# Optimization experiments

Measured on AMD Instinct MI355X. Metric: run time of the kernel, lower is better.

Reference implementation:

```python
import jax, jax.numpy as jnp
import numpy as np

HOP = 128
NFFT = 256
SR = 16000
EPS = 1e-7
MIN_DB = -80.0


def _a_weighting_db():
    # librosa.fft_frequencies + librosa.A_weighting (min_db=-80), computed statically in numpy
    f = np.fft.rfftfreq(NFFT, d=1.0 / SR)  # [NFFT//2+1]
    c = np.array([12194.217, 20.598997, 107.65265, 737.86223]) ** 2.0
    f2 = f ** 2.0
    w = 2.0 + 20.0 * (
        np.log10(c[0])
        + 2.0 * np.log10(np.maximum(f2, 1e-30))
        - np.log10(f2 + c[0])
        - np.log10(f2 + c[1])
        - 0.5 * np.log10(f2 + c[2])
        - 0.5 * np.log10(f2 + c[3])
    )
    return np.maximum(w, MIN_DB).astype(np.float32)


def _loudness(x):
    # x: [B, C, T] -> channel mean -> librosa-style centered STFT (hann, reflect pad)
    x = jnp.mean(x, axis=1)  # [B, T]
    T = x.shape[1]
    pad = NFFT // 2
    xp = jnp.pad(x, ((0, 0), (pad, pad)), mode='reflect')  # [B, T+NFFT]
    n_frames = 1 + T // HOP
    idx = jnp.arange(n_frames)[:, None] * HOP + jnp.arange(NFFT)[None, :]  # [F, NFFT]
    frames = xp[:, idx]  # [B, F, NFFT]
    # periodic hann window (scipy fftbins=True, librosa default)
    win = (0.5 - 0.5 * jnp.cos(2.0 * jnp.pi * jnp.arange(NFFT) / NFFT)).astype(x.dtype)
    spec = jnp.fft.rfft(frames * win, axis=-1)  # [B, F, NFFT//2+1] complex
    log_mag = jnp.log(jnp.abs(spec) + EPS)  # [B, F, NFREQ]
    aw = jnp.asarray(_a_weighting_db())  # [NFREQ]
    # mean over frequency axis, then trailing singleton like original unsqueeze(-1)
    loud = jnp.mean(log_mag + aw[None, None, :], axis=-1)  # [B, F]
    return loud[..., None].astype(jnp.float32)


def setup_inputs() -> dict:
    key = jax.random.key(0)
    x = jax.random.normal(key, (64, 1, 640000), dtype=jnp.float32)
    return {"x": x}


def reference(x):
    return _loudness(x)
```

## Files before the change

### kernel.cpp

```cpp
#include <hip/hip_runtime.h>
#include <math.h>

#define HOP 128
#define T_LEN 640000
#define N_FRAMES 5001
#define N_PAIRS 2501
#define NB 64
#define GPB 16

#define RE_SLOT 18
#define RE_GRP  164
#define IM_SLOT 18
#define IM_GRP  132

typedef float v2f __attribute__((ext_vector_type(2)));

static __device__ __forceinline__ v2f mk2(float a, float b) { v2f r; r.x = a; r.y = b; return r; }
static __device__ __forceinline__ v2f sp(float s) { v2f r; r.x = s; r.y = s; return r; }

static __device__ __forceinline__ float rsum16(float v) {
    v += __int_as_float(__builtin_amdgcn_update_dpp(0, __float_as_int(v), 0xB1, 0xF, 0xF, true));
    v += __int_as_float(__builtin_amdgcn_update_dpp(0, __float_as_int(v), 0x4E, 0xF, 0xF, true));
    v += __int_as_float(__builtin_amdgcn_update_dpp(0, __float_as_int(v), 0x141, 0xF, 0xF, true));
    v += __int_as_float(__builtin_amdgcn_update_dpp(0, __float_as_int(v), 0x140, 0xF, 0xF, true));
    return v;
}

__global__ __launch_bounds__(256) void setup_kernel(float* __restrict__ ws) {
    __shared__ float s_aw[132];
    const int tid = threadIdx.x;
    const float TP = 0.02454369260617026f;
    {
        const int w = tid >> 4, rr = tid & 15;
        float s, c;
        sincosf((float)(rr * w) * TP, &s, &c);
        ((v2f*)ws)[tid] = mk2(c, -s);
    }
    if (tid < 129) {
        const float LG2_10 = 0.30102999566398f;
        float fq = (float)tid * 62.5f;
        float f2 = fq * fq;
        const float a0 = 12194.217f * 12194.217f;
        const float a1 = 20.598997f * 20.598997f;
        const float a2 = 107.65265f * 107.65265f;
        const float a3 = 737.86223f * 737.86223f;
        float w = 2.0f + 20.0f * LG2_10 *
                  (__builtin_amdgcn_logf(a0) + 2.0f * __builtin_amdgcn_logf(fmaxf(f2, 1e-30f))
                 - __builtin_amdgcn_logf(f2 + a0) - __builtin_amdgcn_logf(f2 + a1)
                 - 0.5f * __builtin_amdgcn_logf(f2 + a2) - 0.5f * __builtin_amdgcn_logf(f2 + a3));
        s_aw[tid] = fmaxf(w, -80.0f);
    }
    __syncthreads();
    if (tid < 16) {
        float s = 0.f;
#pragma unroll
        for (int k2 = 0; k2 < 8; ++k2) s += s_aw[tid + 16 * k2];
        ws[512 + tid] = s;
        if (tid == 0) ws[528] = s_aw[128];
    }
}

__global__ __launch_bounds__(256) void loudness_kernel(const float* __restrict__ x,
                                                       float* __restrict__ out,
                                                       const float* __restrict__ ws) {
    constexpr float C16[16] = {
        1.0f,  0.9238795325112867f,  0.7071067811865476f,  0.3826834323650898f,
        0.0f, -0.3826834323650898f, -0.7071067811865476f, -0.9238795325112867f,
       -1.0f, -0.9238795325112867f, -0.7071067811865476f, -0.3826834323650898f,
        0.0f,  0.3826834323650898f,  0.7071067811865476f,  0.9238795325112867f};
    constexpr float S16[16] = {
        0.0f,  0.3826834323650898f,  0.7071067811865476f,  0.9238795325112867f,
        1.0f,  0.9238795325112867f,  0.7071067811865476f,  0.3826834323650898f,
        0.0f, -0.3826834323650898f, -0.7071067811865476f, -0.9238795325112867f,
       -1.0f, -0.9238795325112867f, -0.7071067811865476f, -0.3826834323650898f};
    const float R2  = 0.7071067811865476f;
    const float c1v = 0.9238795325112867f, s1v = 0.3826834323650898f;
    const float c3v = 0.3826834323650898f, s3v = 0.9238795325112867f;
    const float CP8 = 0.9238795325112867f, SP8 = 0.3826834323650898f;
    const float K2  = 1.8477590650225735f;

    __shared__ alignas(16) v2f s_re[16 * RE_GRP];
    __shared__ alignas(16) v2f s_im[16 * IM_GRP];
    __shared__ v2f s_twT[256];

    const int tid = threadIdx.x;
    const int g = tid >> 4;
    const int r = tid & 15;

    s_twT[tid] = ((const v2f*)ws)[tid];
    const float aw8r  = ws[512 + r];
    const float aw128 = ws[528];
    const v2f stp = ((const v2f*)ws)[16 + r];

    float win16[16];
    {
        float cm2 = stp.x;
        float cm1 = stp.x * CP8 + stp.y * SP8;
        win16[0] = 0.5f - 0.5f * cm2;
        win16[1] = 0.5f - 0.5f * cm1;
#pragma unroll
        for (int n = 2; n < 16; ++n) {
            const float c = K2 * cm1 - cm2;
            win16[n] = 0.5f - 0.5f * c;
            cm2 = cm1; cm1 = c;
        }
    }
    __syncthreads();

    const int gp = blockIdx.x * GPB + g;
    const int b  = gp / N_PAIRS;
    const int pp = gp - b * N_PAIRS;
    const int fA = 2 * pp;
    const int fB = (fA < 5000) ? fA + 1 : 5000;
    const int dB = (fB - fA) * HOP;
    const float* __restrict__ xb = x + (size_t)b * T_LEN;

    v2f xw[16];
    const int base = fA * HOP - HOP + r;
    if (pp >= 1 && pp <= 2499) {
        const float* __restrict__ xp = xb + base;
#pragma unroll
        for (int n2 = 0; n2 < 16; ++n2) {
            const int o = 16 * n2;
            xw[n2] = mk2(xp[o], xp[o + dB]) * sp(win16[n2]);
        }
    } else {
#pragma unroll
        for (int n2 = 0; n2 < 16; ++n2) {
            int jA = base + 16 * n2;
            int jB = jA + dB;
            jA = (jA < 0) ? -jA : jA;
            jA = (jA >= T_LEN) ? (2 * T_LEN - 2 - jA) : jA;
            jB = (jB < 0) ? -jB : jB;
            jB = (jB >= T_LEN) ? (2 * T_LEN - 2 - jB) : jB;
            xw[n2] = mk2(xb[jA], xb[jB]) * sp(win16[n2]);
        }
    }

    v2f pv[8], qv[8];
#pragma unroll
    for (int n = 1; n <= 7; ++n) { pv[n] = xw[n] + xw[16 - n]; qv[n] = xw[n] - xw[16 - n]; }
    const v2f bse = xw[0] + xw[8];
    const v2f d08 = xw[0] - xw[8];
    const v2f se  = pv[2] + pv[4] + pv[6];
    const v2f so  = pv[1] + pv[3] + pv[5] + pv[7];
    const v2f r0  = bse + se + so;
    const v2f r8  = bse + se - so;
    v2f rre[8], rim[8];
#pragma unroll
    for (int k1 = 1; k1 <= 7; ++k1) {
        v2f re = (k1 & 1) ? d08 : bse;
        v2f im = sp(0.f);
#pragma unroll
        for (int n = 1; n <= 7; ++n) {
            const int m = (k1 * n) & 15;
            re += pv[n] * sp(C16[m]);
            im -= qv[n] * sp(S16[m]);
        }
        rre[k1] = re;
        rim[k1] = im;
    }

    {
        v2f* __restrict__ reW = &s_re[g * RE_GRP + r];
        v2f* __restrict__ imW = &s_im[g * IM_GRP + r];
        reW[0] = r0;
#pragma unroll
        for (int k = 1; k <= 7; ++k) {
            reW[RE_SLOT * k] = rre[k];
            imW[IM_SLOT * (k - 1)] = rim[k];
        }
        reW[RE_SLOT * 8] = r8;
    }

    const int rp  = (r <= 8) ? r : 16 - r;
    const int rpi = (rp >= 1 && rp <= 7) ? (rp - 1) : 0;
    const float ysgn = (r == 0 || r == 8) ? 0.f : ((r < 8) ? 1.f : -1.f);
    const float4* __restrict__ reCol = (const float4*)&s_re[g * RE_GRP + RE_SLOT * rp];
    const float4* __restrict__ imCol = (const float4*)&s_im[g * IM_GRP + IM_SLOT * rpi];
    const v2f* __restrict__ twp = &s_twT[r];

    v2f bbx[16], bby[16];
#pragma unroll
    for (int j = 0; j < 8; ++j) {
        const float4 R4v = reCol[j];
        const float4 I4v = imCol[j];
        {
            const int w = 2 * j;
            const v2f tw = twp[16 * w];
            const v2f xx = mk2(R4v.x, R4v.y);
            const v2f yy = mk2(I4v.x, I4v.y) * sp(ysgn);
            bbx[w] = xx * sp(tw.x) - yy * sp(tw.y);
            bby[w] = xx * sp(tw.y) + yy * sp(tw.x);
        }
        {
            const int w = 2 * j + 1;
            const v2f tw = twp[16 * w];
            const v2f xx = mk2(R4v.z, R4v.w);
            const v2f yy = mk2(I4v.z, I4v.w) * sp(ysgn);
            bbx[w] = xx * sp(tw.x) - yy * sp(tw.y);
            bby[w] = xx * sp(tw.y) + yy * sp(tw.x);
        }
    }

#pragma unroll
    for (int j = 0; j < 8; ++j) {
        const v2f ux = bbx[j], uy = bby[j], vx = bbx[j + 8], vy = bby[j + 8];
        bbx[j] = ux + vx; bby[j] = uy + vy;
        const v2f dx = ux - vx, dy = uy - vy;
        v2f ox, oy;
        if      (j == 0) { ox = dx;                              oy = dy; }
        else if (j == 1) { ox =  dx * sp(c1v) + dy * sp(s1v);    oy =  dy * sp(c1v) - dx * sp(s1v); }
        else if (j == 2) { ox = (dx + dy) * sp(R2);              oy = (dy - dx) * sp(R2); }
        else if (j == 3) { ox =  dx * sp(c3v) + dy * sp(s3v);    oy =  dy * sp(c3v) - dx * sp(s3v); }
        else if (j == 4) { ox = dy;                              oy = sp(0.f) - dx; }
        else if (j == 5) { ox = dy * sp(s3v) - dx * sp(c3v);     oy = sp(0.f) - dy * sp(c3v) - dx * sp(s3v); }
        else if (j == 6) { ox = (dy - dx) * sp(R2);              oy = sp(0.f) - (dx + dy) * sp(R2); }
        else             { ox = dy * sp(s1v) - dx * sp(c1v);     oy = sp(0.f) - dy * sp(c1v) - dx * sp(s1v); }
        bbx[j + 8] = ox; bby[j + 8] = oy;
    }
#pragma unroll
    for (int h = 0; h <= 8; h += 8) {
#pragma unroll
        for (int j = 0; j < 4; ++j) {
            const v2f ux = bbx[h + j], uy = bby[h + j], vx = bbx[h + j + 4], vy = bby[h + j + 4];
            bbx[h + j] = ux + vx; bby[h + j] = uy + vy;
            const v2f dx = ux - vx, dy = uy - vy;
            v2f ox, oy;
            if      (j == 0) { ox = dx;                  oy = dy; }
            else if (j == 1) { ox = (dx + dy) * sp(R2);  oy = (dy - dx) * sp(R2); }
            else if (j == 2) { ox = dy;                  oy = sp(0.f) - dx; }
            else             { ox = (dy - dx) * sp(R2);  oy = sp(0.f) - (dx + dy) * sp(R2); }
            bbx[h + j + 4] = ox; bby[h + j + 4] = oy;
        }
    }
#pragma unroll
    for (int gg = 0; gg < 16; gg += 4) {
        {
            const v2f ux = bbx[gg], uy = bby[gg], vx = bbx[gg + 2], vy = bby[gg + 2];
            bbx[gg] = ux + vx;     bby[gg] = uy + vy;
            bbx[gg + 2] = ux - vx; bby[gg + 2] = uy - vy;
        }
        {
            const v2f ux = bbx[gg + 1], uy = bby[gg + 1], vx = bbx[gg + 3], vy = bby[gg + 3];
            bbx[gg + 1] = ux + vx; bby[gg + 1] = uy + vy;
            const v2f dx = ux - vx, dy = uy - vy;
            bbx[gg + 3] = dy; bby[gg + 3] = sp(0.f) - dx;
        }
    }

    const float HALF_LN2 = 0.34657359027997264f;
    v2f m2[8];
#pragma unroll
    for (int t = 0; t < 8; ++t) {
        const v2f Yx = bbx[2 * t] + bbx[2 * t + 1];
        const v2f Yy = bby[2 * t] + bby[2 * t + 1];
        m2[t] = Yx * Yx + Yy * Yy + sp(1e-14f);
    }
    const v2f P0 = m2[0] * m2[1], P1 = m2[2] * m2[3], P2 = m2[4] * m2[5], P3 = m2[6] * m2[7];
    const float lA = __builtin_amdgcn_logf(P0.x) + __builtin_amdgcn_logf(P1.x)
                   + __builtin_amdgcn_logf(P2.x) + __builtin_amdgcn_logf(P3.x);
    const float lB = __builtin_amdgcn_logf(P0.y) + __builtin_amdgcn_logf(P1.y)
                   + __builtin_amdgcn_logf(P2.y) + __builtin_amdgcn_logf(P3.y);
    v2f ssum = sp(HALF_LN2) * mk2(lA, lB) + sp(aw8r);

    const v2f d0 = bbx[0] - bbx[1];
    if (r == 0) {
        ssum += sp(HALF_LN2) * mk2(__builtin_amdgcn_logf(d0.x * d0.x + 1e-14f),
                                   __builtin_amdgcn_logf(d0.y * d0.y + 1e-14f))
              + sp(aw128);
    }

    ssum.x = rsum16(ssum.x);
    ssum.y = rsum16(ssum.y);

    if (r == 0) {
        out[b * N_FRAMES + fA] = ssum.x * (1.0f / 129.0f);
        out[b * N_FRAMES + fB] = ssum.y * (1.0f / 129.0f);
    }
}

extern "C" void kernel_launch(void* const* d_in, const int* in_sizes, int n_in,
                              void* d_out, int out_size, void* d_ws, size_t ws_size,
                              hipStream_t stream) {
    const float* x = (const float*)d_in[0];
    float* out = (float*)d_out;
    float* ws = (float*)d_ws;
    setup_kernel<<<1, 256, 0, stream>>>(ws);
    loudness_kernel<<<(NB * N_PAIRS) / GPB, 256, 0, stream>>>(x, out, ws);
}
```

Measured before the change: 55.48 us.

## Merge shared spectra buffers, fold twiddles in registers, swizzle blocks across XCDs

The block's twiddle table is dropped from shared memory. Twiddles are now applied before the transpose by a per-thread sincos and a rotation recurrence, and the twiddle for the high-half lanes is folded into constant C16/S16 multiplies. The real and imaginary spectra share one reused shared buffer written in two phases, which cuts the LDS footprint. A launch-bounds occupancy hint of 5 and an XCD-aware block-index swizzle for L2 locality are also added. The two-phase reuse and the recurrence-based twiddles may add numeric error and instruction dependencies, and the reuse has no __syncthreads between phases (each 16-lane group is assumed to sit within one wavefront).

```diff
diff --git a/kernel.cpp b/kernel.cpp
--- a/kernel.cpp
+++ b/kernel.cpp
@@ -7,11 +7,10 @@
 #define N_PAIRS 2501
 #define NB 64
 #define GPB 16
-
-#define RE_SLOT 18
-#define RE_GRP  164
-#define IM_SLOT 18
-#define IM_GRP  132
+#define NWG ((NB * N_PAIRS) / GPB)
+
+#define SLOT 18
+#define GRP  162
 
 typedef float v2f __attribute__((ext_vector_type(2)));
 
@@ -29,13 +28,6 @@
 __global__ __launch_bounds__(256) void setup_kernel(float* __restrict__ ws) {
     __shared__ float s_aw[132];
     const int tid = threadIdx.x;
-    const float TP = 0.02454369260617026f;
-    {
-        const int w = tid >> 4, rr = tid & 15;
-        float s, c;
-        sincosf((float)(rr * w) * TP, &s, &c);
-        ((v2f*)ws)[tid] = mk2(c, -s);
-    }
     if (tid < 129) {
         const float LG2_10 = 0.30102999566398f;
         float fq = (float)tid * 62.5f;
@@ -55,14 +47,14 @@
         float s = 0.f;
 #pragma unroll
         for (int k2 = 0; k2 < 8; ++k2) s += s_aw[tid + 16 * k2];
-        ws[512 + tid] = s;
-        if (tid == 0) ws[528] = s_aw[128];
+        ws[tid] = s;
+        if (tid == 0) ws[16] = s_aw[128];
     }
 }
 
-__global__ __launch_bounds__(256) void loudness_kernel(const float* __restrict__ x,
-                                                       float* __restrict__ out,
-                                                       const float* __restrict__ ws) {
+__global__ __launch_bounds__(256, 5) void loudness_kernel(const float* __restrict__ x,
+                                                          float* __restrict__ out,
+                                                          const float* __restrict__ ws) {
     constexpr float C16[16] = {
         1.0f,  0.9238795325112867f,  0.7071067811865476f,  0.3826834323650898f,
         0.0f, -0.3826834323650898f, -0.7071067811865476f, -0.9238795325112867f,
@@ -79,18 +71,34 @@
     const float CP8 = 0.9238795325112867f, SP8 = 0.3826834323650898f;
     const float K2  = 1.8477590650225735f;
 
-    __shared__ alignas(16) v2f s_re[16 * RE_GRP];
-    __shared__ alignas(16) v2f s_im[16 * IM_GRP];
-    __shared__ v2f s_twT[256];
+    __shared__ alignas(16) v2f s_sp[16 * GRP];
 
     const int tid = threadIdx.x;
     const int g = tid >> 4;
     const int r = tid & 15;
 
-    s_twT[tid] = ((const v2f*)ws)[tid];
-    const float aw8r  = ws[512 + r];
-    const float aw128 = ws[528];
-    const v2f stp = ((const v2f*)ws)[16 + r];
+    const int orig = blockIdx.x;
+    const int xcd = orig & 7, idx = orig >> 3;
+    const int q = NWG >> 3, rem = NWG & 7;
+    const int swz = (xcd < rem) ? xcd * (q + 1) + idx
+                                : rem * (q + 1) + (xcd - rem) * q + idx;
+
+    const int gp = swz * GPB + g;
+    const int b  = gp / N_PAIRS;
+    const int pp = gp - b * N_PAIRS;
+    const int fA = 2 * pp;
+    const int fB = (fA < 5000) ? fA + 1 : 5000;
+    const int dB = (fB - fA) * HOP;
+    const float* __restrict__ xb = x + (size_t)b * T_LEN;
+
+    v2f stp;
+    {
+        float s, c;
+        sincosf((float)r * 0.02454369260617026f, &s, &c);
+        stp = mk2(c, -s);
+    }
+    const float aw8r  = ws[r];
+    const float aw128 = ws[16];
 
     float win16[16];
     {
@@ -105,15 +113,6 @@
             cm2 = cm1; cm1 = c;
         }
     }
-    __syncthreads();
-
-    const int gp = blockIdx.x * GPB + g;
-    const int b  = gp / N_PAIRS;
-    const int pp = gp - b * N_PAIRS;
-    const int fA = 2 * pp;
-    const int fB = (fA < 5000) ? fA + 1 : 5000;
-    const int dB = (fB - fA) * HOP;
-    const float* __restrict__ xb = x + (size_t)b * T_LEN;
 
     v2f xw[16];
     const int base = fA * HOP - HOP + r;
@@ -161,45 +160,66 @@
         rim[k1] = im;
     }
 
+    v2f* __restrict__ wbase = &s_sp[g * GRP];
+    v2f Zim[9];
     {
-        v2f* __restrict__ reW = &s_re[g * RE_GRP + r];
-        v2f* __restrict__ imW = &s_im[g * IM_GRP + r];
-        reW[0] = r0;
-#pragma unroll
-        for (int k = 1; k <= 7; ++k) {
-            reW[RE_SLOT * k] = rre[k];
-            imW[IM_SLOT * (k - 1)] = rim[k];
-        }
-        reW[RE_SLOT * 8] = r8;
-    }
-
-    const int rp  = (r <= 8) ? r : 16 - r;
-    const int rpi = (rp >= 1 && rp <= 7) ? (rp - 1) : 0;
-    const float ysgn = (r == 0 || r == 8) ? 0.f : ((r < 8) ? 1.f : -1.f);
-    const float4* __restrict__ reCol = (const float4*)&s_re[g * RE_GRP + RE_SLOT * rp];
-    const float4* __restrict__ imCol = (const float4*)&s_im[g * IM_GRP + IM_SLOT * rpi];
-    const v2f* __restrict__ twp = &s_twT[r];
-
+        wbase[r] = r0;
+        float twx = stp.x, twy = stp.y;
+#pragma unroll
+        for (int k = 1; k <= 8; ++k) {
+            const v2f rr = (k < 8) ? rre[k] : r8;
+            const v2f ri = (k < 8) ? rim[k] : sp(0.f);
+            wbase[SLOT * k + r] = rr * sp(twx) - ri * sp(twy);
+            Zim[k]              = rr * sp(twy) + ri * sp(twx);
+            if (k < 8) {
+                const float nx = twx * stp.x - twy * stp.y;
+                const float ny = twx * stp.y + twy * stp.x;
+                twx = nx; twy = ny;
+            }
+        }
+    }
+    __builtin_amdgcn_sched_barrier(0);
+
+    const int rp = (r <= 8) ? r : 16 - r;
+    const float4* __restrict__ reCol = (const float4*)&s_sp[g * GRP + SLOT * rp];
     v2f bbx[16], bby[16];
 #pragma unroll
     for (int j = 0; j < 8; ++j) {
-        const float4 R4v = reCol[j];
-        const float4 I4v = imCol[j];
-        {
-            const int w = 2 * j;
-            const v2f tw = twp[16 * w];
-            const v2f xx = mk2(R4v.x, R4v.y);
-            const v2f yy = mk2(I4v.x, I4v.y) * sp(ysgn);
-            bbx[w] = xx * sp(tw.x) - yy * sp(tw.y);
-            bby[w] = xx * sp(tw.y) + yy * sp(tw.x);
-        }
-        {
-            const int w = 2 * j + 1;
-            const v2f tw = twp[16 * w];
-            const v2f xx = mk2(R4v.z, R4v.w);
-            const v2f yy = mk2(I4v.z, I4v.w) * sp(ysgn);
-            bbx[w] = xx * sp(tw.x) - yy * sp(tw.y);
-            bby[w] = xx * sp(tw.y) + yy * sp(tw.x);
+        const float4 Z4 = reCol[j];
+        const v2f Zx0 = mk2(Z4.x, Z4.y), Zx1 = mk2(Z4.z, Z4.w);
+        const int w0 = 2 * j, w1 = 2 * j + 1;
+        if (r <= 8) {
+            bbx[w0] = Zx0;
+            bbx[w1] = Zx1;
+        } else {
+            bbx[w0] = Zx0 * sp(C16[w0]);
+            bby[w0] = sp(0.f) - Zx0 * sp(S16[w0]);
+            bbx[w1] = Zx1 * sp(C16[w1]);
+            bby[w1] = sp(0.f) - Zx1 * sp(S16[w1]);
+        }
+    }
+    __builtin_amdgcn_sched_barrier(0);
+
+#pragma unroll
+    for (int k = 1; k <= 8; ++k) wbase[SLOT * (k - 1) + r] = Zim[k];
+    __builtin_amdgcn_sched_barrier(0);
+
+    const int rpi = (r == 0) ? 0 : ((r <= 8) ? r - 1 : 15 - r);
+    const float im0 = (r == 0) ? 0.f : 1.f;
+    const float4* __restrict__ imCol = (const float4*)&s_sp[g * GRP + SLOT * rpi];
+#pragma unroll
+    for (int j = 0; j < 8; ++j) {
+        const float4 Z4 = imCol[j];
+        const v2f Zy0 = mk2(Z4.x, Z4.y), Zy1 = mk2(Z4.z, Z4.w);
+        const int w0 = 2 * j, w1 = 2 * j + 1;
+        if (r <= 8) {
+            bby[w0] = Zy0 * sp(im0);
+            bby[w1] = Zy1 * sp(im0);
+        } else {
+            bbx[w0] -= Zy0 * sp(S16[w0]);
+            bby[w0] -= Zy0 * sp(C16[w0]);
+            bbx[w1] -= Zy1 * sp(S16[w1]);
+            bby[w1] -= Zy1 * sp(C16[w1]);
         }
     }
 
@@ -287,5 +307,5 @@
     float* out = (float*)d_out;
     float* ws = (float*)d_ws;
     setup_kernel<<<1, 256, 0, stream>>>(ws);
-    loudness_kernel<<<(NB * N_PAIRS) / GPB, 256, 0, stream>>>(x, out, ws);
+    loudness_kernel<<<NWG, 256, 0, stream>>>(x, out, ws);
 }
```

After: 147.2 us. 165% more time.

## Swizzle shared spectrum layout, precompute window, drop syncthreads, remap blocks per XCD

Applied to the files above, without the earlier changes.

Replaces the padded separate real/imag shared buffers with one XOR-swizzled 256-entry buffer per group, so the transposed float4 reads avoid bank conflicts without padding. The Hann window is now precomputed in the setup kernel and loaded as float4s, and twiddles are read directly from global memory instead of being staged in LDS. This removes the block-wide __syncthreads at kernel start. Block indices are also remapped so consecutive work lands on the same XCD, aiming for better L2 locality. The cost is extra global/L1 loads for twiddles and window per thread.

```diff
diff --git a/kernel.cpp b/kernel.cpp
--- a/kernel.cpp
+++ b/kernel.cpp
@@ -7,11 +7,7 @@
 #define N_PAIRS 2501
 #define NB 64
 #define GPB 16
-
-#define RE_SLOT 18
-#define RE_GRP  164
-#define IM_SLOT 18
-#define IM_GRP  132
+#define NWG ((NB * N_PAIRS) / GPB)
 
 typedef float v2f __attribute__((ext_vector_type(2)));
 
@@ -30,12 +26,6 @@
     __shared__ float s_aw[132];
     const int tid = threadIdx.x;
     const float TP = 0.02454369260617026f;
-    {
-        const int w = tid >> 4, rr = tid & 15;
-        float s, c;
-        sincosf((float)(rr * w) * TP, &s, &c);
-        ((v2f*)ws)[tid] = mk2(c, -s);
-    }
     if (tid < 129) {
         const float LG2_10 = 0.30102999566398f;
         float fq = (float)tid * 62.5f;
@@ -50,13 +40,21 @@
                  - 0.5f * __builtin_amdgcn_logf(f2 + a2) - 0.5f * __builtin_amdgcn_logf(f2 + a3));
         s_aw[tid] = fmaxf(w, -80.0f);
     }
+    ws[32 + (tid & 15) * 16 + (tid >> 4)] = 0.5f - 0.5f * cosf((float)tid * TP);
+    {
+        const int w = tid >> 4, rr = tid & 15;
+        float s, c;
+        sincosf((float)(w * rr) * TP, &s, &c);
+        ws[288 + 2 * tid]     = c;
+        ws[288 + 2 * tid + 1] = -s;
+    }
     __syncthreads();
     if (tid < 16) {
         float s = 0.f;
 #pragma unroll
         for (int k2 = 0; k2 < 8; ++k2) s += s_aw[tid + 16 * k2];
-        ws[512 + tid] = s;
-        if (tid == 0) ws[528] = s_aw[128];
+        ws[tid] = s;
+        if (tid == 0) ws[16] = s_aw[128];
     }
 }
 
@@ -76,44 +74,39 @@
     const float R2  = 0.7071067811865476f;
     const float c1v = 0.9238795325112867f, s1v = 0.3826834323650898f;
     const float c3v = 0.3826834323650898f, s3v = 0.9238795325112867f;
-    const float CP8 = 0.9238795325112867f, SP8 = 0.3826834323650898f;
-    const float K2  = 1.8477590650225735f;
-
-    __shared__ alignas(16) v2f s_re[16 * RE_GRP];
-    __shared__ alignas(16) v2f s_im[16 * IM_GRP];
-    __shared__ v2f s_twT[256];
+
+    __shared__ alignas(16) v2f s_sp[16 * 256];
 
     const int tid = threadIdx.x;
     const int g = tid >> 4;
     const int r = tid & 15;
 
-    s_twT[tid] = ((const v2f*)ws)[tid];
-    const float aw8r  = ws[512 + r];
-    const float aw128 = ws[528];
-    const v2f stp = ((const v2f*)ws)[16 + r];
-
-    float win16[16];
-    {
-        float cm2 = stp.x;
-        float cm1 = stp.x * CP8 + stp.y * SP8;
-        win16[0] = 0.5f - 0.5f * cm2;
-        win16[1] = 0.5f - 0.5f * cm1;
-#pragma unroll
-        for (int n = 2; n < 16; ++n) {
-            const float c = K2 * cm1 - cm2;
-            win16[n] = 0.5f - 0.5f * c;
-            cm2 = cm1; cm1 = c;
-        }
-    }
-    __syncthreads();
-
-    const int gp = blockIdx.x * GPB + g;
+    const int orig = blockIdx.x;
+    const int xcd = orig & 7, idx = orig >> 3;
+    const int q = NWG >> 3, rem = NWG & 7;
+    const int swz = (xcd < rem) ? xcd * (q + 1) + idx
+                                : rem * (q + 1) + (xcd - rem) * q + idx;
+
+    const int gp = swz * GPB + g;
     const int b  = gp / N_PAIRS;
     const int pp = gp - b * N_PAIRS;
     const int fA = 2 * pp;
     const int fB = (fA < 5000) ? fA + 1 : 5000;
     const int dB = (fB - fA) * HOP;
     const float* __restrict__ xb = x + (size_t)b * T_LEN;
+
+    const float aw8r  = ws[r];
+    const float aw128 = ws[16];
+    float win16[16];
+    {
+        const float4* __restrict__ wp = (const float4*)(ws + 32 + r * 16);
+#pragma unroll
+        for (int c4 = 0; c4 < 4; ++c4) {
+            const float4 t = wp[c4];
+            win16[4 * c4 + 0] = t.x; win16[4 * c4 + 1] = t.y;
+            win16[4 * c4 + 2] = t.z; win16[4 * c4 + 3] = t.w;
+        }
+    }
 
     v2f xw[16];
     const int base = fA * HOP - HOP + r;
@@ -162,32 +155,35 @@
     }
 
     {
-        v2f* __restrict__ reW = &s_re[g * RE_GRP + r];
-        v2f* __restrict__ imW = &s_im[g * IM_GRP + r];
-        reW[0] = r0;
-#pragma unroll
-        for (int k = 1; k <= 7; ++k) {
-            reW[RE_SLOT * k] = rre[k];
-            imW[IM_SLOT * (k - 1)] = rim[k];
-        }
-        reW[RE_SLOT * 8] = r8;
+        v2f* __restrict__ wb = &s_sp[g * 256];
+        const int wq2 = r >> 1, wh = r & 1;
+        wb[0 * 16 + 2 * (wq2 ^ 0) + wh] = r0;
+#pragma unroll
+        for (int k = 1; k <= 7; ++k)
+            wb[k * 16 + 2 * (wq2 ^ (k & 7)) + wh] = rre[k];
+        wb[8 * 16 + 2 * (wq2 ^ 0) + wh] = r8;
+#pragma unroll
+        for (int k = 1; k <= 7; ++k)
+            wb[(8 + k) * 16 + 2 * (wq2 ^ ((8 + k) & 7)) + wh] = rim[k];
     }
 
     const int rp  = (r <= 8) ? r : 16 - r;
     const int rpi = (rp >= 1 && rp <= 7) ? (rp - 1) : 0;
+    const int sIm = 9 + rpi;
     const float ysgn = (r == 0 || r == 8) ? 0.f : ((r < 8) ? 1.f : -1.f);
-    const float4* __restrict__ reCol = (const float4*)&s_re[g * RE_GRP + RE_SLOT * rp];
-    const float4* __restrict__ imCol = (const float4*)&s_im[g * IM_GRP + IM_SLOT * rpi];
-    const v2f* __restrict__ twp = &s_twT[r];
+    const float4* __restrict__ f4 = (const float4*)&s_sp[g * 256];
+    const int reB = rp * 8,  reQ = rp & 7;
+    const int imB = sIm * 8, imQ = sIm & 7;
+    const v2f* __restrict__ twg = ((const v2f*)(ws + 288)) + r;
 
     v2f bbx[16], bby[16];
 #pragma unroll
     for (int j = 0; j < 8; ++j) {
-        const float4 R4v = reCol[j];
-        const float4 I4v = imCol[j];
+        const float4 R4v = f4[reB + (j ^ reQ)];
+        const float4 I4v = f4[imB + (j ^ imQ)];
         {
             const int w = 2 * j;
-            const v2f tw = twp[16 * w];
+            const v2f tw = twg[16 * w];
             const v2f xx = mk2(R4v.x, R4v.y);
             const v2f yy = mk2(I4v.x, I4v.y) * sp(ysgn);
             bbx[w] = xx * sp(tw.x) - yy * sp(tw.y);
@@ -195,7 +191,7 @@
         }
         {
             const int w = 2 * j + 1;
-            const v2f tw = twp[16 * w];
+            const v2f tw = twg[16 * w];
             const v2f xx = mk2(R4v.z, R4v.w);
             const v2f yy = mk2(I4v.z, I4v.w) * sp(ysgn);
             bbx[w] = xx * sp(tw.x) - yy * sp(tw.y);
@@ -287,5 +283,5 @@
     float* out = (float*)d_out;
     float* ws = (float*)d_ws;
     setup_kernel<<<1, 256, 0, stream>>>(ws);
-    loudness_kernel<<<(NB * N_PAIRS) / GPB, 256, 0, stream>>>(x, out, ws);
-}
+    loudness_kernel<<<NWG, 256, 0, stream>>>(x, out, ws);
+}
```

After: 58.70 us. +5.8%, slower.
